# Performance work log

Measured on AMD Instinct MI355X. Metric: run time of the kernel, lower is better.

Reference implementation:

```python
import jax, jax.numpy as jnp
import numpy as np
from jax import lax

SIZE = 4096
NUM_CONVS = 5
FC_IN = 16 * 16
EPS = 1e-5


def _forward(x_real, x_imag, mag_kernel, phase_kernel, conv_w, conv_b,
             bn_gamma, bn_beta, bn_mean, bn_var, prelu_a,
             fc5_w, fc5_b, ln_gamma, ln_beta, prelu5_a, fc6_w, fc6_b):
    # KernelModule51: magnitude/phase scaling -> recombine -> ifftshift -> ifft2 -> real
    mag = jnp.sqrt(x_real * x_real + x_imag * x_imag) * mag_kernel      # (1,S,S)
    ph = jnp.arctan2(x_imag, x_real) * phase_kernel                     # (1,S,S)
    combined = lax.complex(mag * jnp.cos(ph), mag * jnp.sin(ph))        # m*exp(i*p)
    x = jnp.fft.ifft2(jnp.fft.ifftshift(combined, axes=(-2, -1)), axes=(-2, -1)).real
    x = x[:, None, :, :]  # (1,1,S,S) NCHW

    for i in range(NUM_CONVS):
        x = lax.conv_general_dilated(x, conv_w[i], window_strides=(3, 3), padding='VALID',
                                     dimension_numbers=('NCHW', 'OIHW', 'NCHW'))
        x = x + conv_b[i][None, :, None, None]
        scale = (bn_gamma[i] * lax.rsqrt(bn_var[i] + EPS))[None, :, None, None]
        shift = (bn_beta[i] - bn_gamma[i] * bn_mean[i] * lax.rsqrt(bn_var[i] + EPS))[None, :, None, None]
        x = x * scale + shift
        x = jnp.where(x >= 0, x, prelu_a[i] * x)

    x = x.reshape(x.shape[0], -1)                                       # (1, FC_IN)
    x = x @ fc5_w + fc5_b                                               # (1, 82)
    mu = jnp.mean(x, axis=-1, keepdims=True)
    var = jnp.mean((x - mu) ** 2, axis=-1, keepdims=True)
    x = (x - mu) * lax.rsqrt(var + EPS) * ln_gamma + ln_beta
    x = jnp.where(x >= 0, x, prelu5_a * x)
    return x @ fc6_w + fc6_b                                            # (1, 5)


def setup_inputs() -> dict:
    key = jax.random.key(0)
    ks = jax.random.split(key, 9)
    f32 = jnp.float32
    return {
        'x_real': jax.random.normal(ks[0], (1, SIZE, SIZE), f32),
        'x_imag': jax.random.normal(ks[1], (1, SIZE, SIZE), f32),
        'mag_kernel': jax.random.normal(ks[2], (1, SIZE, SIZE), f32),
        'phase_kernel': jax.random.normal(ks[3], (1, SIZE, SIZE), f32),
        'conv_w': jax.random.normal(ks[4], (NUM_CONVS, 1, 1, 3, 3), f32) * 0.33,
        'conv_b': jax.random.normal(ks[5], (NUM_CONVS, 1), f32) * 0.1,
        'bn_gamma': jnp.ones((NUM_CONVS, 1), f32),
        'bn_beta': jnp.zeros((NUM_CONVS, 1), f32),
        'bn_mean': jnp.zeros((NUM_CONVS, 1), f32),
        'bn_var': jnp.ones((NUM_CONVS, 1), f32),
        'prelu_a': jnp.full((NUM_CONVS,), 0.25, f32),
        'fc5_w': jax.random.normal(ks[6], (FC_IN, 82), f32) * (1.0 / np.sqrt(FC_IN)),
        'fc5_b': jnp.zeros((82,), f32),
        'ln_gamma': jnp.ones((82,), f32),
        'ln_beta': jnp.zeros((82,), f32),
        'prelu5_a': jnp.asarray(0.25, f32),
        'fc6_w': jax.random.normal(ks[7], (82, 5), f32) * (1.0 / np.sqrt(82.0)),
        'fc6_b': jnp.zeros((5,), f32),
    }


def reference(x_real, x_imag, mag_kernel, phase_kernel, conv_w, conv_b,
              bn_gamma, bn_beta, bn_mean, bn_var, prelu_a,
              fc5_w, fc5_b, ln_gamma, ln_beta, prelu5_a, fc6_w, fc6_b):
    return _forward(x_real, x_imag, mag_kernel, phase_kernel, conv_w, conv_b,
                    bn_gamma, bn_beta, bn_mean, bn_var, prelu_a,
                    fc5_w, fc5_b, ln_gamma, ln_beta, prelu5_a, fc6_w, fc6_b)
```

## Files before the change

kernel.cpp:

```cpp
#include <hip/hip_runtime.h>
#include <hip/hip_fp16.h>
#include <math.h>

#define N 4096
#define TPB 256
#define PI2_F 6.283185307179586f
#define PAD(i) ((i) + ((i) >> 4))

__device__ __forceinline__ float2 cmul(float2 a, float2 b) {
    return make_float2(a.x * b.x - a.y * b.y, a.x * b.y + a.y * b.x);
}
__device__ __forceinline__ float2 cadd(float2 a, float2 b) { return make_float2(a.x + b.x, a.y + b.y); }
__device__ __forceinline__ float2 csub(float2 a, float2 b) { return make_float2(a.x - b.x, a.y - b.y); }
__device__ __forceinline__ float2 muli(float2 a) { return make_float2(-a.y, a.x); }

__device__ __forceinline__ float fast_atan2f(float y, float x) {
    float ax = fabsf(x), ay = fabsf(y);
    float mx = fmaxf(ax, ay), mn = fminf(ax, ay);
    float t = mn * __builtin_amdgcn_rcpf(fmaxf(mx, 1e-37f));
    float s = t * t;
    float r = fmaf(s, fmaf(s, fmaf(s, fmaf(s, 0.0208351f, -0.0851330f),
                                    0.1801410f), -0.3302995f), 0.9998660f) * t;
    if (ay > ax) r = 1.5707963267948966f - r;
    if (x < 0.0f) r = 3.1415926535897932f - r;
    return copysignf(r, y);
}

__device__ __forceinline__ void ifft16(float2 v[16]) {
    const float C1 = 0.9238795325112867f, S1 = 0.3826834323650898f;
    const float C2 = 0.7071067811865476f;
    float2 y[16];
    #pragma unroll
    for (int t = 0; t < 4; ++t) {
        float2 a0 = v[t], a1 = v[t + 4], a2 = v[t + 8], a3 = v[t + 12];
        float2 t0 = cadd(a0, a2), t1 = csub(a0, a2);
        float2 t2 = cadd(a1, a3), t3 = muli(csub(a1, a3));
        float2 c0 = cadd(t0, t2), c1 = cadd(t1, t3);
        float2 c2 = csub(t0, t2), c3 = csub(t1, t3);
        if (t == 0) {
            y[0] = c0; y[1] = c1; y[2] = c2; y[3] = c3;
        } else if (t == 1) {
            y[4] = c0;
            y[5] = cmul(c1, make_float2(C1, S1));
            y[6] = cmul(c2, make_float2(C2, C2));
            y[7] = cmul(c3, make_float2(S1, C1));
        } else if (t == 2) {
            y[8] = c0;
            y[9]  = cmul(c1, make_float2(C2, C2));
            y[10] = muli(c2);
            y[11] = cmul(c3, make_float2(-C2, C2));
        } else {
            y[12] = c0;
            y[13] = cmul(c1, make_float2(S1, C1));
            y[14] = cmul(c2, make_float2(-C2, C2));
            y[15] = cmul(c3, make_float2(-C1, -S1));
        }
    }
    #pragma unroll
    for (int t = 0; t < 4; ++t) {
        float2 a0 = y[t], a1 = y[t + 4], a2 = y[t + 8], a3 = y[t + 12];
        float2 t0 = cadd(a0, a2), t1 = csub(a0, a2);
        float2 t2 = cadd(a1, a3), t3 = muli(csub(a1, a3));
        v[t]      = cadd(t0, t2);
        v[t + 4]  = cadd(t1, t3);
        v[t + 8]  = csub(t0, t2);
        v[t + 12] = csub(t1, t3);
    }
}

__global__ __launch_bounds__(TPB, 4) void k_fft_rows_fused(
    const float* __restrict__ xr, const float* __restrict__ xi,
    const float* __restrict__ mk, const float* __restrict__ pk,
    __half2* __restrict__ out)
{
    __shared__ float2 lds[4096 + 256];
    const int t = threadIdx.x;
    const size_t base = (size_t)blockIdx.x * N;
    float2 v[16];

    #pragma unroll
    for (int q = 0; q < 16; ++q) {
        int idx = t + 256 * q;
        float a = xr[base + idx];
        float b = xi[base + idx];
        float mag = sqrtf(a * a + b * b) * mk[base + idx];
        float ph  = fast_atan2f(b, a) * pk[base + idx];
        float s, c;
        __sincosf(ph, &s, &c);
        v[q] = make_float2(mag * c, mag * s);
    }

    ifft16(v);
    {
        float s1, c1;
        __sincosf(PI2_F * (float)t * (1.0f / 4096.0f), &s1, &c1);
        float2 w1 = make_float2(c1, s1);
        float2 w = make_float2(1.0f, 0.0f);
        #pragma unroll
        for (int p = 0; p < 16; ++p) {
            lds[PAD(16 * t + p)] = cmul(v[p], w);
            w = cmul(w, w1);
        }
    }
    __syncthreads();
    #pragma unroll
    for (int q = 0; q < 16; ++q) v[q] = lds[PAD(t + 256 * q)];
    __syncthreads();

    ifft16(v);
    {
        int j = t >> 4, k = t & 15;
        float s1, c1;
        __sincosf(PI2_F * (float)j * (1.0f / 256.0f), &s1, &c1);
        float2 w1 = make_float2(c1, s1);
        float2 w = make_float2(1.0f, 0.0f);
        int dbase = j * 256 + k;
        #pragma unroll
        for (int p = 0; p < 16; ++p) {
            lds[PAD(dbase + 16 * p)] = cmul(v[p], w);
            w = cmul(w, w1);
        }
    }
    __syncthreads();
    #pragma unroll
    for (int q = 0; q < 16; ++q) v[q] = lds[PAD(t + 256 * q)];

    ifft16(v);
    const float S = 1.0f / 4096.0f;
    #pragma unroll
    for (int p = 0; p < 16; ++p)
        out[base + t + 256 * p] = __floats2half2_rn(v[p].x * S, v[p].y * S);
}

__global__ void k_transpose(const unsigned int* __restrict__ in,
                            unsigned int* __restrict__ out)
{
    __shared__ unsigned int tile[32][33];
    const int bx = blockIdx.x * 32, by = blockIdx.y * 32;
    const int tx = threadIdx.x, ty = threadIdx.y;
    #pragma unroll
    for (int k = 0; k < 4; ++k)
        tile[ty + k * 8][tx] = in[(size_t)(by + ty + k * 8) * N + bx + tx];
    __syncthreads();
    #pragma unroll
    for (int k = 0; k < 4; ++k)
        out[(size_t)(bx + ty + k * 8) * N + by + tx] = tile[tx][ty + k * 8];
}

__global__ __launch_bounds__(TPB, 4) void k_fft_rows_final(
    const __half2* __restrict__ in, float* __restrict__ out)
{
    __shared__ float2 lds[4096 + 256];
    const int t = threadIdx.x;
    const int row = blockIdx.x;
    const size_t base = (size_t)row * N;
    float2 v[16];

    #pragma unroll
    for (int q = 0; q < 16; ++q) v[q] = __half22float2(in[base + t + 256 * q]);

    ifft16(v);
    {
        float s1, c1;
        __sincosf(PI2_F * (float)t * (1.0f / 4096.0f), &s1, &c1);
        float2 w1 = make_float2(c1, s1);
        float2 w = make_float2(1.0f, 0.0f);
        #pragma unroll
        for (int p = 0; p < 16; ++p) {
            lds[PAD(16 * t + p)] = cmul(v[p], w);
            w = cmul(w, w1);
        }
    }
    __syncthreads();
    #pragma unroll
    for (int q = 0; q < 16; ++q) v[q] = lds[PAD(t + 256 * q)];
    __syncthreads();

    ifft16(v);
    {
        int j = t >> 4, k = t & 15;
        float s1, c1;
        __sincosf(PI2_F * (float)j * (1.0f / 256.0f), &s1, &c1);
        float2 w1 = make_float2(c1, s1);
        float2 w = make_float2(1.0f, 0.0f);
        int dbase = j * 256 + k;
        #pragma unroll
        for (int p = 0; p < 16; ++p) {
            lds[PAD(dbase + 16 * p)] = cmul(v[p], w);
            w = cmul(w, w1);
        }
    }
    __syncthreads();
    #pragma unroll
    for (int q = 0; q < 16; ++q) v[q] = lds[PAD(t + 256 * q)];

    ifft16(v);

    const float scale = 1.0f / 4096.0f;
    const float sgn = ((row + t) & 1) ? -scale : scale;
    #pragma unroll
    for (int p = 0; p < 16; ++p) out[base + t + 256 * p] = v[p].x * sgn;
}

__device__ __forceinline__ float conv_bn_prelu(
    const float* __restrict__ in, int win, int r, int c,
    const float* __restrict__ cw, const float* __restrict__ cb,
    const float* __restrict__ bg, const float* __restrict__ bb,
    const float* __restrict__ bm, const float* __restrict__ bv,
    const float* __restrict__ pa, int layer)
{
    const float* w = cw + layer * 9;
    float acc = 0.0f;
    #pragma unroll
    for (int di = 0; di < 3; ++di)
        #pragma unroll
        for (int dj = 0; dj < 3; ++dj)
            acc += in[(size_t)(3 * r + dj) * win + (3 * c + di)] * w[di * 3 + dj];
    float g  = bg[layer];
    float rs = rsqrtf(bv[layer] + 1e-5f);
    float scale = g * rs;
    float shift = bb[layer] - g * bm[layer] * rs;
    float v = (acc + cb[layer]) * scale + shift;
    float a = pa[layer];
    return v >= 0.0f ? v : a * v;
}

__global__ void k_conv(const float* __restrict__ in, float* __restrict__ out,
                       int win, int wout,
                       const float* __restrict__ cw, const float* __restrict__ cb,
                       const float* __restrict__ bg, const float* __restrict__ bb,
                       const float* __restrict__ bm, const float* __restrict__ bv,
                       const float* __restrict__ pa, int layer)
{
    int idx = blockIdx.x * blockDim.x + threadIdx.x;
    if (idx >= wout * wout) return;
    int r = idx / wout, c = idx % wout;
    out[idx] = conv_bn_prelu(in, win, r, c, cw, cb, bg, bb, bm, bv, pa, layer);
}

__global__ __launch_bounds__(1024) void k_tail(
    const float* __restrict__ c3img,
    const float* __restrict__ cw, const float* __restrict__ cb,
    const float* __restrict__ bg, const float* __restrict__ bb,
    const float* __restrict__ bm, const float* __restrict__ bv,
    const float* __restrict__ pa,
    const float* __restrict__ w5, const float* __restrict__ b5,
    const float* __restrict__ lg, const float* __restrict__ lb,
    const float* __restrict__ p5a,
    const float* __restrict__ w6, const float* __restrict__ b6,
    float* __restrict__ out)
{
    __shared__ float s4[2500];
    __shared__ float s5[256];
    __shared__ float sx[256];
    __shared__ float h[82];
    __shared__ float red[2];
    const int tid = threadIdx.x;

    for (int idx = tid; idx < 2500; idx += 1024) {
        int r = idx / 50, c = idx % 50;
        s4[idx] = conv_bn_prelu(c3img, 151, r, c, cw, cb, bg, bb, bm, bv, pa, 3);
    }
    __syncthreads();

    if (tid < 256) {
        int r = tid >> 4, c = tid & 15;
        const float* w = cw + 4 * 9;
        float acc = 0.0f;
        #pragma unroll
        for (int di = 0; di < 3; ++di)
            #pragma unroll
            for (int dj = 0; dj < 3; ++dj)
                acc += s4[(3 * r + dj) * 50 + (3 * c + di)] * w[di * 3 + dj];
        float g  = bg[4];
        float rs = rsqrtf(bv[4] + 1e-5f);
        float v = (acc + cb[4]) * (g * rs) + (bb[4] - g * bm[4] * rs);
        float a = pa[4];
        s5[tid] = v >= 0.0f ? v : a * v;
    }
    __syncthreads();

    if (tid < 256) {
        int m = tid >> 4, n = tid & 15;
        sx[tid] = s5[n * 16 + m];
    }
    __syncthreads();

    if (tid < 82) {
        float acc = b5[tid];
        for (int k = 0; k < 256; ++k) acc += sx[k] * w5[k * 82 + tid];
        h[tid] = acc;
    }
    __syncthreads();
    if (tid == 0) {
        float mu = 0.0f;
        for (int o = 0; o < 82; ++o) mu += h[o];
        mu *= (1.0f / 82.0f);
        float var = 0.0f;
        for (int o = 0; o < 82; ++o) { float d = h[o] - mu; var += d * d; }
        var *= (1.0f / 82.0f);
        red[0] = mu;
        red[1] = rsqrtf(var + 1e-5f);
    }
    __syncthreads();
    if (tid < 82) {
        float v = (h[tid] - red[0]) * red[1] * lg[tid] + lb[tid];
        float a = p5a[0];
        h[tid] = v >= 0.0f ? v : a * v;
    }
    __syncthreads();
    if (tid < 5) {
        float acc = b6[tid];
        for (int o = 0; o < 82; ++o) acc += h[o] * w6[o * 5 + tid];
        out[tid] = acc;
    }
}

extern "C" void kernel_launch(void* const* d_in, const int* in_sizes, int n_in,
                              void* d_out, int out_size, void* d_ws, size_t ws_size,
                              hipStream_t stream)
{
    const float* xr  = (const float*)d_in[0];
    const float* xi  = (const float*)d_in[1];
    const float* mk  = (const float*)d_in[2];
    const float* pk  = (const float*)d_in[3];
    const float* cw  = (const float*)d_in[4];
    const float* cb  = (const float*)d_in[5];
    const float* bg  = (const float*)d_in[6];
    const float* bb  = (const float*)d_in[7];
    const float* bm  = (const float*)d_in[8];
    const float* bv  = (const float*)d_in[9];
    const float* pa  = (const float*)d_in[10];
    const float* w5  = (const float*)d_in[11];
    const float* b5  = (const float*)d_in[12];
    const float* lg  = (const float*)d_in[13];
    const float* lb  = (const float*)d_in[14];
    const float* p5a = (const float*)d_in[15];
    const float* w6  = (const float*)d_in[16];
    const float* b6  = (const float*)d_in[17];
    float* outp = (float*)d_out;

    char* ws = (char*)d_ws;
    const size_t Q = (size_t)64 * 1024 * 1024;
    __half2* A = (__half2*)ws;
    __half2* B = (__half2*)(ws + Q);
    float*  ximg = (float*)(ws + 2 * Q);
    float* c1 = (float*)ws;
    float* c2 = c1 + 1365 * 1365;
    float* c3 = c2 + 455 * 455;

    k_fft_rows_fused<<<N, TPB, 0, stream>>>(xr, xi, mk, pk, A);
    k_transpose<<<dim3(N / 32, N / 32), dim3(32, 8), 0, stream>>>(
        (const unsigned int*)A, (unsigned int*)B);
    k_fft_rows_final<<<N, TPB, 0, stream>>>(B, ximg);

    k_conv<<<(1365 * 1365 + 255) / 256, 256, 0, stream>>>(ximg, c1, 4096, 1365,
        cw, cb, bg, bb, bm, bv, pa, 0);
    k_conv<<<(455 * 455 + 255) / 256, 256, 0, stream>>>(c1, c2, 1365, 455,
        cw, cb, bg, bb, bm, bv, pa, 1);
    k_conv<<<(151 * 151 + 255) / 256, 256, 0, stream>>>(c2, c3, 455, 151,
        cw, cb, bg, bb, bm, bv, pa, 2);

    k_tail<<<1, 1024, 0, stream>>>(c3, cw, cb, bg, bb, bm, bv, pa,
                                   w5, b5, lg, lb, p5a, w6, b6, outp);
}
```

Before: 378.4 us.

## Store FFT LDS exchanges and real image in fp16, raise occupancy bound

Both row-FFT kernels now keep their inter-stage LDS buffers as half2 instead of float2, which halves shared memory per block so launch bounds can request 8 blocks per SIMD instead of 4. The final FFT writes the real image as fp16, and a dedicated first conv kernel reads that half image, cutting the 64MB float write and read to 32MB. It also factors BN/PReLU into a helper. This trades extra precision loss inside the FFT stages for less LDS and global traffic, and the higher occupancy target may force register spills.

```diff
diff --git a/kernel.cpp b/kernel.cpp
--- a/kernel.cpp
+++ b/kernel.cpp
@@ -68,12 +68,12 @@
     }
 }
 
-__global__ __launch_bounds__(TPB, 4) void k_fft_rows_fused(
+__global__ __launch_bounds__(TPB, 8) void k_fft_rows_fused(
     const float* __restrict__ xr, const float* __restrict__ xi,
     const float* __restrict__ mk, const float* __restrict__ pk,
     __half2* __restrict__ out)
 {
-    __shared__ float2 lds[4096 + 256];
+    __shared__ __half2 lds[4096 + 256];
     const int t = threadIdx.x;
     const size_t base = (size_t)blockIdx.x * N;
     float2 v[16];
@@ -98,13 +98,14 @@
         float2 w = make_float2(1.0f, 0.0f);
         #pragma unroll
         for (int p = 0; p < 16; ++p) {
-            lds[PAD(16 * t + p)] = cmul(v[p], w);
+            float2 z = cmul(v[p], w);
+            lds[PAD(16 * t + p)] = __floats2half2_rn(z.x, z.y);
             w = cmul(w, w1);
         }
     }
     __syncthreads();
     #pragma unroll
-    for (int q = 0; q < 16; ++q) v[q] = lds[PAD(t + 256 * q)];
+    for (int q = 0; q < 16; ++q) v[q] = __half22float2(lds[PAD(t + 256 * q)]);
     __syncthreads();
 
     ifft16(v);
@@ -117,13 +118,14 @@
         int dbase = j * 256 + k;
         #pragma unroll
         for (int p = 0; p < 16; ++p) {
-            lds[PAD(dbase + 16 * p)] = cmul(v[p], w);
+            float2 z = cmul(v[p], w);
+            lds[PAD(dbase + 16 * p)] = __floats2half2_rn(z.x, z.y);
             w = cmul(w, w1);
         }
     }
     __syncthreads();
     #pragma unroll
-    for (int q = 0; q < 16; ++q) v[q] = lds[PAD(t + 256 * q)];
+    for (int q = 0; q < 16; ++q) v[q] = __half22float2(lds[PAD(t + 256 * q)]);
 
     ifft16(v);
     const float S = 1.0f / 4096.0f;
@@ -147,10 +149,10 @@
         out[(size_t)(bx + ty + k * 8) * N + by + tx] = tile[tx][ty + k * 8];
 }
 
-__global__ __launch_bounds__(TPB, 4) void k_fft_rows_final(
-    const __half2* __restrict__ in, float* __restrict__ out)
-{
-    __shared__ float2 lds[4096 + 256];
+__global__ __launch_bounds__(TPB, 8) void k_fft_rows_final(
+    const __half2* __restrict__ in, __half* __restrict__ out)
+{
+    __shared__ __half2 lds[4096 + 256];
     const int t = threadIdx.x;
     const int row = blockIdx.x;
     const size_t base = (size_t)row * N;
@@ -167,13 +169,14 @@
         float2 w = make_float2(1.0f, 0.0f);
         #pragma unroll
         for (int p = 0; p < 16; ++p) {
-            lds[PAD(16 * t + p)] = cmul(v[p], w);
+            float2 z = cmul(v[p], w);
+            lds[PAD(16 * t + p)] = __floats2half2_rn(z.x, z.y);
             w = cmul(w, w1);
         }
     }
     __syncthreads();
     #pragma unroll
-    for (int q = 0; q < 16; ++q) v[q] = lds[PAD(t + 256 * q)];
+    for (int q = 0; q < 16; ++q) v[q] = __half22float2(lds[PAD(t + 256 * q)]);
     __syncthreads();
 
     ifft16(v);
@@ -186,43 +189,54 @@
         int dbase = j * 256 + k;
         #pragma unroll
         for (int p = 0; p < 16; ++p) {
-            lds[PAD(dbase + 16 * p)] = cmul(v[p], w);
+            float2 z = cmul(v[p], w);
+            lds[PAD(dbase + 16 * p)] = __floats2half2_rn(z.x, z.y);
             w = cmul(w, w1);
         }
     }
     __syncthreads();
     #pragma unroll
-    for (int q = 0; q < 16; ++q) v[q] = lds[PAD(t + 256 * q)];
+    for (int q = 0; q < 16; ++q) v[q] = __half22float2(lds[PAD(t + 256 * q)]);
 
     ifft16(v);
 
     const float scale = 1.0f / 4096.0f;
     const float sgn = ((row + t) & 1) ? -scale : scale;
     #pragma unroll
-    for (int p = 0; p < 16; ++p) out[base + t + 256 * p] = v[p].x * sgn;
-}
-
-__device__ __forceinline__ float conv_bn_prelu(
-    const float* __restrict__ in, int win, int r, int c,
-    const float* __restrict__ cw, const float* __restrict__ cb,
-    const float* __restrict__ bg, const float* __restrict__ bb,
-    const float* __restrict__ bm, const float* __restrict__ bv,
-    const float* __restrict__ pa, int layer)
-{
-    const float* w = cw + layer * 9;
-    float acc = 0.0f;
-    #pragma unroll
-    for (int di = 0; di < 3; ++di)
-        #pragma unroll
-        for (int dj = 0; dj < 3; ++dj)
-            acc += in[(size_t)(3 * r + dj) * win + (3 * c + di)] * w[di * 3 + dj];
+    for (int p = 0; p < 16; ++p)
+        out[base + t + 256 * p] = __float2half_rn(v[p].x * sgn);
+}
+
+__device__ __forceinline__ float bn_prelu(float acc,
+    const float* __restrict__ cb, const float* __restrict__ bg,
+    const float* __restrict__ bb, const float* __restrict__ bm,
+    const float* __restrict__ bv, const float* __restrict__ pa, int layer)
+{
     float g  = bg[layer];
     float rs = rsqrtf(bv[layer] + 1e-5f);
-    float scale = g * rs;
-    float shift = bb[layer] - g * bm[layer] * rs;
-    float v = (acc + cb[layer]) * scale + shift;
+    float v = (acc + cb[layer]) * (g * rs) + (bb[layer] - g * bm[layer] * rs);
     float a = pa[layer];
     return v >= 0.0f ? v : a * v;
+}
+
+__global__ void k_conv_h0(const __half* __restrict__ in, float* __restrict__ out,
+                          const float* __restrict__ cw, const float* __restrict__ cb,
+                          const float* __restrict__ bg, const float* __restrict__ bb,
+                          const float* __restrict__ bm, const float* __restrict__ bv,
+                          const float* __restrict__ pa)
+{
+    const int wout = 1365, win = 4096;
+    int idx = blockIdx.x * blockDim.x + threadIdx.x;
+    if (idx >= wout * wout) return;
+    int r = idx / wout, c = idx % wout;
+    const float* w = cw;
+    float acc = 0.0f;
+    #pragma unroll
+    for (int di = 0; di < 3; ++di)
+        #pragma unroll
+        for (int dj = 0; dj < 3; ++dj)
+            acc += __half2float(in[(size_t)(3 * r + dj) * win + (3 * c + di)]) * w[di * 3 + dj];
+    out[idx] = bn_prelu(acc, cb, bg, bb, bm, bv, pa, 0);
 }
 
 __global__ void k_conv(const float* __restrict__ in, float* __restrict__ out,
@@ -235,7 +249,14 @@
     int idx = blockIdx.x * blockDim.x + threadIdx.x;
     if (idx >= wout * wout) return;
     int r = idx / wout, c = idx % wout;
-    out[idx] = conv_bn_prelu(in, win, r, c, cw, cb, bg, bb, bm, bv, pa, layer);
+    const float* w = cw + layer * 9;
+    float acc = 0.0f;
+    #pragma unroll
+    for (int di = 0; di < 3; ++di)
+        #pragma unroll
+        for (int dj = 0; dj < 3; ++dj)
+            acc += in[(size_t)(3 * r + dj) * win + (3 * c + di)] * w[di * 3 + dj];
+    out[idx] = bn_prelu(acc, cb, bg, bb, bm, bv, pa, layer);
 }
 
 __global__ __launch_bounds__(1024) void k_tail(
@@ -259,7 +280,14 @@
 
     for (int idx = tid; idx < 2500; idx += 1024) {
         int r = idx / 50, c = idx % 50;
-        s4[idx] = conv_bn_prelu(c3img, 151, r, c, cw, cb, bg, bb, bm, bv, pa, 3);
+        const float* w = cw + 3 * 9;
+        float acc = 0.0f;
+        #pragma unroll
+        for (int di = 0; di < 3; ++di)
+            #pragma unroll
+            for (int dj = 0; dj < 3; ++dj)
+                acc += c3img[(size_t)(3 * r + dj) * 151 + (3 * c + di)] * w[di * 3 + dj];
+        s4[idx] = bn_prelu(acc, cb, bg, bb, bm, bv, pa, 3);
     }
     __syncthreads();
 
@@ -272,11 +300,7 @@
             #pragma unroll
             for (int dj = 0; dj < 3; ++dj)
                 acc += s4[(3 * r + dj) * 50 + (3 * c + di)] * w[di * 3 + dj];
-        float g  = bg[4];
-        float rs = rsqrtf(bv[4] + 1e-5f);
-        float v = (acc + cb[4]) * (g * rs) + (bb[4] - g * bm[4] * rs);
-        float a = pa[4];
-        s5[tid] = v >= 0.0f ? v : a * v;
+        s5[tid] = bn_prelu(acc, cb, bg, bb, bm, bv, pa, 4);
     }
     __syncthreads();
 
@@ -344,7 +368,7 @@
     const size_t Q = (size_t)64 * 1024 * 1024;
     __half2* A = (__half2*)ws;
     __half2* B = (__half2*)(ws + Q);
-    float*  ximg = (float*)(ws + 2 * Q);
+    __half*  ximg = (__half*)(ws + 2 * Q);
     float* c1 = (float*)ws;
     float* c2 = c1 + 1365 * 1365;
     float* c3 = c2 + 455 * 455;
@@ -354,8 +378,8 @@
         (const unsigned int*)A, (unsigned int*)B);
     k_fft_rows_final<<<N, TPB, 0, stream>>>(B, ximg);
 
-    k_conv<<<(1365 * 1365 + 255) / 256, 256, 0, stream>>>(ximg, c1, 4096, 1365,
-        cw, cb, bg, bb, bm, bv, pa, 0);
+    k_conv_h0<<<(1365 * 1365 + 255) / 256, 256, 0, stream>>>(ximg, c1,
+        cw, cb, bg, bb, bm, bv, pa);
     k_conv<<<(455 * 455 + 255) / 256, 256, 0, stream>>>(c1, c2, 1365, 455,
         cw, cb, bg, bb, bm, bv, pa, 1);
     k_conv<<<(151 * 151 + 255) / 256, 256, 0, stream>>>(c2, c3, 455, 151,
```

Result: slower. 546.0 us (+44.3%).
